# Kernel tuning notes

Measured on AMD Instinct MI355X. Metric: run time of the kernel, lower is better.

## Reference

```python
import jax, jax.numpy as jnp
from jax import lax
import numpy as np


def _gaussian_blur5(x):
    # x: [B,1,H,W]; torchvision gaussian_blur(kernel_size=5) default sigma = 0.3*((5-1)*0.5-1)+0.8 = 1.1
    sigma = 1.1
    r = jnp.arange(5, dtype=x.dtype) - 2.0
    k = jnp.exp(-(r * r) / (2.0 * sigma * sigma))
    k = k / k.sum()
    dn = ('NCHW', 'OIHW', 'NCHW')
    xp = jnp.pad(x, ((0, 0), (0, 0), (2, 2), (0, 0)), mode='reflect')
    x = lax.conv_general_dilated(xp, k.reshape(1, 1, 5, 1), (1, 1), 'VALID', dimension_numbers=dn)
    xp = jnp.pad(x, ((0, 0), (0, 0), (0, 0), (2, 2)), mode='reflect')
    return lax.conv_general_dilated(xp, k.reshape(1, 1, 1, 5), (1, 1), 'VALID', dimension_numbers=dn)


def setup_inputs() -> dict:
    key = jax.random.key(0)
    k1, k2, k3 = jax.random.split(key, 3)
    T, B, D, heads = 2, 32, 768, 12
    H_t, W_t, H_s, W_s = 14, 14, 96, 96
    template_patches = jax.random.normal(k1, (T, B, H_t * W_t, D), dtype=jnp.float32)
    template_annos = jax.random.uniform(k2, (T, B, 4), dtype=jnp.float32)
    search_key = jax.random.normal(k3, (B, heads, H_s * W_s + 1, D // heads), dtype=jnp.float32)
    return {'template_patches': template_patches, 'template_annos': template_annos,
            'search_key': search_key, 'H_t': H_t, 'W_t': W_t, 'H_s': H_s, 'W_s': W_s}


def reference(template_patches, template_annos, search_key, H_t, W_t, H_s, W_s):
    T, B, Nt, D = template_patches.shape
    heads = search_key.shape[1]
    hd = D // heads
    # --- vectorized patch-mask construction from normalized [x,y,w,h] boxes ---
    x1 = jnp.floor(template_annos[..., 0] * W_t).astype(jnp.int32)  # int() trunc == floor for >=0
    y1 = jnp.floor(template_annos[..., 1] * H_t).astype(jnp.int32)
    x2 = jnp.floor((template_annos[..., 0] + template_annos[..., 2]) * W_t).astype(jnp.int32)
    y2 = jnp.floor((template_annos[..., 1] + template_annos[..., 3]) * H_t).astype(jnp.int32)
    rows = jnp.arange(H_t)[None, None, :, None]
    cols = jnp.arange(W_t)[None, None, None, :]
    mask = ((rows >= y1[..., None, None]) & (rows < y2[..., None, None]) &
            (cols >= x1[..., None, None]) & (cols < x2[..., None, None]))
    mask = mask.reshape(T, B, Nt, 1).astype(template_patches.dtype)
    # --- masked-mean prototypes, averaged over templates ---
    count = mask.sum(axis=2)                                   # [T,B,1]
    protos = (template_patches * mask).sum(axis=2) / (count + 1e-6)  # [T,B,D]
    proto = protos.mean(axis=0)                                # [B,D]
    # --- per-head cross-attention scores against search keys (CLS stripped) ---
    proto_h = proto.reshape(B, heads, hd)
    skp = search_key[:, :, 1:, :]                              # [B,heads,Ns,hd]
    attn = jnp.einsum('bhd,bhnd->bhn', proto_h, skp) * (hd ** -0.5)
    track = attn.mean(axis=1).reshape(B, 1, H_s, W_s)
    track = _gaussian_blur5(track)
    prob = jax.nn.softmax(track.reshape(B, -1), axis=-1).reshape(B, H_s, W_s)
    # --- integral-image sliding-window box scoring ---
    im = jnp.cumsum(jnp.cumsum(prob, axis=-1), axis=-2)
    p = jnp.pad(im, ((0, 0), (1, 0), (1, 0)))
    Dv = p[:, H_t:, W_t:]
    Cv = p[:, H_t:, :-W_t]
    Bv = p[:, :-H_t, W_t:]
    Av = p[:, :-H_t, :-W_t]
    sum_map = Dv - Bv - Cv + Av                                # [B, H_s-H_t+1, W_s-W_t+1]
    flat = sum_map.reshape(B, -1)
    idx = jnp.argmax(flat, axis=1)
    confidence = jnp.max(flat, axis=1)
    best_y = idx // sum_map.shape[2]
    best_x = idx % sum_map.shape[2]
    win_w = jnp.full((B,), W_t, dtype=jnp.int32)
    win_h = jnp.full((B,), H_t, dtype=jnp.int32)
    return best_x, best_y, win_w, win_h, confidence, prob
```

## Files before the change

kernel.cpp:

```cpp
#include <hip/hip_runtime.h>
#include <math.h>

#define TT 2
#define BB 32
#define DD 768
#define HEADS 12
#define HD 64
#define HT 14
#define WT 14
#define HS 96
#define WS 96
#define NS (HS*WS)
#define NSK (NS+1)
#define SMW (WS-WT+1)
#define SMH (HS-HT+1)

__global__ __launch_bounds__(256) void proto_kernel(
    const float* __restrict__ patches, const float* __restrict__ annos,
    float* __restrict__ protos) {
  const int dc = blockIdx.x, t = blockIdx.y, b = blockIdx.z;
  const int d = dc * 256 + threadIdx.x;

  const float* an = annos + (t * BB + b) * 4;
  const float ax = an[0], ay = an[1], aw = an[2], ah = an[3];
  const int x1 = (int)floorf(ax * (float)WT);
  const int y1 = (int)floorf(ay * (float)HT);
  const int x2 = (int)floorf((ax + aw) * (float)WT);
  const int y2 = (int)floorf((ay + ah) * (float)HT);
  const int cx2 = min(x2, WT), cy2 = min(y2, HT);
  const int cw = max(cx2 - x1, 0), ch = max(cy2 - y1, 0);
  const float count = (float)(cw * ch);

  float s = 0.f;
  const float* base = patches + ((size_t)(t * BB + b)) * (HT*WT) * DD + d;
  for (int r = y1; r < cy2; ++r)
    for (int c = x1; c < cx2; ++c)
      s += base[(r * WT + c) * DD];

  protos[(size_t)(t * BB + b) * DD + d] = s / (count + 1e-6f);
}

__global__ __launch_bounds__(256) void attn_kernel(
    const float* __restrict__ sk, const float* __restrict__ protos,
    float* __restrict__ track) {
  const int b = blockIdx.y;
  const int tid = threadIdx.x;
  const int lane16 = tid & 15;
  const int grp = tid >> 4;
  const int n0 = blockIdx.x * 64;

  float4 pr[HEADS];
  const float4* p0 = (const float4*)(protos + (size_t)b * DD);
  const float4* p1 = (const float4*)(protos + (size_t)(BB + b) * DD);
  #pragma unroll
  for (int h = 0; h < HEADS; ++h) {
    float4 a = p0[h * 16 + lane16];
    float4 c = p1[h * 16 + lane16];
    pr[h] = make_float4(0.5f * (a.x + c.x), 0.5f * (a.y + c.y),
                        0.5f * (a.z + c.z), 0.5f * (a.w + c.w));
  }

  const float* skb = sk + (size_t)b * HEADS * NSK * HD;
  float acc[4] = {0.f, 0.f, 0.f, 0.f};
  #pragma unroll
  for (int j = 0; j < 4; ++j) {
    const int row = n0 + 16 * j + grp;
    const float4* base = (const float4*)(skb + (size_t)(row + 1) * HD) + lane16;
    #pragma unroll
    for (int h = 0; h < HEADS; ++h) {
      float4 v = base[h * (NSK * HD / 4)];
      acc[j] += v.x * pr[h].x + v.y * pr[h].y + v.z * pr[h].z + v.w * pr[h].w;
    }
  }

  #pragma unroll
  for (int j = 0; j < 4; ++j) {
    #pragma unroll
    for (int s = 1; s < 16; s <<= 1)
      acc[j] += __shfl_xor(acc[j], s, 64);
    if (lane16 == 0)
      track[(size_t)b * NS + n0 + 16 * j + grp] = acc[j] * (1.0f / 96.0f);
  }
}

__device__ __forceinline__ int reflect96(int p) {
  return p < 0 ? -p : (p > 95 ? 190 - p : p);
}

__global__ __launch_bounds__(256) void post_kernel(
    const float* __restrict__ track, float* __restrict__ out) {
  __shared__ float P[97 * 97];
  __shared__ float red[256];
  __shared__ int redi[256];
  const int b = blockIdx.x, tid = threadIdx.x;

  const float e2 = expf(-4.0f / (2.0f * 1.1f * 1.1f));
  const float e1 = expf(-1.0f / (2.0f * 1.1f * 1.1f));
  const float wsum = 2.f * e2 + 2.f * e1 + 1.f;
  const float w0 = e2 / wsum, w1 = e1 / wsum, w2 = 1.f / wsum;

  const float* tr = track + (size_t)b * NS;

  for (int i = tid; i < NS; i += 256) {
    const int r = i / WS, c = i % WS;
    float acc = w2 * tr[r * WS + c];
    acc += w1 * (tr[reflect96(r - 1) * WS + c] + tr[reflect96(r + 1) * WS + c]);
    acc += w0 * (tr[reflect96(r - 2) * WS + c] + tr[reflect96(r + 2) * WS + c]);
    P[r * 97 + c] = acc;
  }
  __syncthreads();

  float vals[36];
  #pragma unroll
  for (int k = 0; k < 36; ++k) {
    const int i = tid + k * 256;
    const int r = i / WS, c = i % WS;
    float acc = w2 * P[r * 97 + c];
    acc += w1 * (P[r * 97 + reflect96(c - 1)] + P[r * 97 + reflect96(c + 1)]);
    acc += w0 * (P[r * 97 + reflect96(c - 2)] + P[r * 97 + reflect96(c + 2)]);
    vals[k] = acc;
  }
  __syncthreads();

  float lm = -1e30f;
  #pragma unroll
  for (int k = 0; k < 36; ++k) lm = fmaxf(lm, vals[k]);
  red[tid] = lm; __syncthreads();
  for (int s = 128; s > 0; s >>= 1) {
    if (tid < s) red[tid] = fmaxf(red[tid], red[tid + s]);
    __syncthreads();
  }
  const float m = red[0]; __syncthreads();

  float ls = 0.f;
  #pragma unroll
  for (int k = 0; k < 36; ++k) { vals[k] = expf(vals[k] - m); ls += vals[k]; }
  red[tid] = ls; __syncthreads();
  for (int s = 128; s > 0; s >>= 1) {
    if (tid < s) red[tid] += red[tid + s];
    __syncthreads();
  }
  const float inv = 1.0f / red[0]; __syncthreads();

  float* prob_out = out + 5 * BB + (size_t)b * NS;
  #pragma unroll
  for (int k = 0; k < 36; ++k) {
    const int i = tid + k * 256;
    const int r = i / WS, c = i % WS;
    const float p = vals[k] * inv;
    prob_out[i] = p;
    P[(r + 1) * 97 + (c + 1)] = p;
  }
  for (int i = tid; i < 97; i += 256) { P[i] = 0.f; P[i * 97] = 0.f; }
  __syncthreads();

  if (tid < 96) {
    const int c = tid + 1;
    float run = P[97 + c];
    for (int r = 2; r < 97; ++r) { run += P[r * 97 + c]; P[r * 97 + c] = run; }
  }
  __syncthreads();
  if (tid < 96) {
    const int r = tid + 1;
    float run = 0.f;
    for (int c = 1; c < 97; ++c) { run += P[r * 97 + c]; P[r * 97 + c] = run; }
  }
  __syncthreads();

  float bv = -1e30f; int bi = 0x7fffffff;
  for (int i = tid; i < SMH * SMW; i += 256) {
    const int y = i / SMW, x = i % SMW;
    const float v = P[(y + HT) * 97 + (x + WT)] - P[y * 97 + (x + WT)]
                  - P[(y + HT) * 97 + x] + P[y * 97 + x];
    if (v > bv || (v == bv && i < bi)) { bv = v; bi = i; }
  }
  red[tid] = bv; redi[tid] = bi; __syncthreads();
  for (int s = 128; s > 0; s >>= 1) {
    if (tid < s) {
      const float ov = red[tid + s]; const int oi = redi[tid + s];
      if (ov > red[tid] || (ov == red[tid] && oi < redi[tid])) {
        red[tid] = ov; redi[tid] = oi;
      }
    }
    __syncthreads();
  }

  if (tid == 0) {
    const int idx = redi[0];
    out[0 * BB + b] = (float)(idx % SMW);
    out[1 * BB + b] = (float)(idx / SMW);
    out[2 * BB + b] = (float)WT;
    out[3 * BB + b] = (float)HT;
    out[4 * BB + b] = red[0];
  }
}

extern "C" void kernel_launch(void* const* d_in, const int* in_sizes, int n_in,
                              void* d_out, int out_size, void* d_ws, size_t ws_size,
                              hipStream_t stream) {
  (void)in_sizes; (void)n_in; (void)out_size; (void)ws_size;
  const float* patches = (const float*)d_in[0];
  const float* annos   = (const float*)d_in[1];
  const float* sk      = (const float*)d_in[2];
  float* ws = (float*)d_ws;
  float* protos = ws;
  float* track  = ws + (size_t)TT * BB * DD;
  float* out = (float*)d_out;

  proto_kernel<<<dim3(DD / 256, TT, BB), 256, 0, stream>>>(patches, annos, protos);
  attn_kernel<<<dim3(NS / 64, BB), 256, 0, stream>>>(sk, protos, track);
  post_kernel<<<BB, 256, 0, stream>>>(track, out);
}
```

Measured before the change: 1.199 ms.

## Parallelize attention per head with contiguous streaming and reduce heads in post kernel

Result: slower. 1.241 ms (+3.4%).

```diff
diff --git a/kernel.cpp b/kernel.cpp
--- a/kernel.cpp
+++ b/kernel.cpp
@@ -15,6 +15,10 @@
 #define SMW (WS-WT+1)
 #define SMH (HS-HT+1)
 
+#define CHUNKS 12
+#define CROWS (NS / CHUNKS)
+#define CITERS (CROWS / 16)
+
 __global__ __launch_bounds__(256) void proto_kernel(
     const float* __restrict__ patches, const float* __restrict__ annos,
     float* __restrict__ protos) {
@@ -40,46 +44,34 @@
   protos[(size_t)(t * BB + b) * DD + d] = s / (count + 1e-6f);
 }
 
-__global__ __launch_bounds__(256) void attn_kernel(
+__global__ __launch_bounds__(256, 8) void attn_kernel(
     const float* __restrict__ sk, const float* __restrict__ protos,
-    float* __restrict__ track) {
-  const int b = blockIdx.y;
+    float* __restrict__ track_h) {
+  const int chunk = blockIdx.x, h = blockIdx.y, b = blockIdx.z;
   const int tid = threadIdx.x;
   const int lane16 = tid & 15;
   const int grp = tid >> 4;
-  const int n0 = blockIdx.x * 64;
-
-  float4 pr[HEADS];
-  const float4* p0 = (const float4*)(protos + (size_t)b * DD);
-  const float4* p1 = (const float4*)(protos + (size_t)(BB + b) * DD);
-  #pragma unroll
-  for (int h = 0; h < HEADS; ++h) {
-    float4 a = p0[h * 16 + lane16];
-    float4 c = p1[h * 16 + lane16];
-    pr[h] = make_float4(0.5f * (a.x + c.x), 0.5f * (a.y + c.y),
-                        0.5f * (a.z + c.z), 0.5f * (a.w + c.w));
-  }
-
-  const float* skb = sk + (size_t)b * HEADS * NSK * HD;
-  float acc[4] = {0.f, 0.f, 0.f, 0.f};
-  #pragma unroll
-  for (int j = 0; j < 4; ++j) {
-    const int row = n0 + 16 * j + grp;
-    const float4* base = (const float4*)(skb + (size_t)(row + 1) * HD) + lane16;
-    #pragma unroll
-    for (int h = 0; h < HEADS; ++h) {
-      float4 v = base[h * (NSK * HD / 4)];
-      acc[j] += v.x * pr[h].x + v.y * pr[h].y + v.z * pr[h].z + v.w * pr[h].w;
-    }
-  }
-
-  #pragma unroll
-  for (int j = 0; j < 4; ++j) {
-    #pragma unroll
-    for (int s = 1; s < 16; s <<= 1)
-      acc[j] += __shfl_xor(acc[j], s, 64);
-    if (lane16 == 0)
-      track[(size_t)b * NS + n0 + 16 * j + grp] = acc[j] * (1.0f / 96.0f);
+
+  const float4* p0 = (const float4*)(protos + (size_t)b * DD + h * HD);
+  const float4* p1 = (const float4*)(protos + (size_t)(BB + b) * DD + h * HD);
+  const float4 a = p0[lane16], c = p1[lane16];
+  const float4 pr = make_float4(0.5f * (a.x + c.x), 0.5f * (a.y + c.y),
+                                0.5f * (a.z + c.z), 0.5f * (a.w + c.w));
+
+  const int row0 = chunk * CROWS;
+  const float4* base =
+      (const float4*)(sk + ((size_t)(b * HEADS + h) * NSK + 1 + row0) * HD);
+  float* outb = track_h + (size_t)(b * HEADS + h) * NS + row0;
+
+  #pragma unroll 8
+  for (int i = 0; i < CITERS; ++i) {
+    const float4 v = base[i * 256 + tid];
+    float r = v.x * pr.x + v.y * pr.y + v.z * pr.z + v.w * pr.w;
+    r += __shfl_xor(r, 1, 64);
+    r += __shfl_xor(r, 2, 64);
+    r += __shfl_xor(r, 4, 64);
+    r += __shfl_xor(r, 8, 64);
+    if (lane16 == 0) outb[i * 16 + grp] = r;
   }
 }
 
@@ -88,8 +80,9 @@
 }
 
 __global__ __launch_bounds__(256) void post_kernel(
-    const float* __restrict__ track, float* __restrict__ out) {
+    const float* __restrict__ track_h, float* __restrict__ out) {
   __shared__ float P[97 * 97];
+  __shared__ float Q[96 * 96];
   __shared__ float red[256];
   __shared__ int redi[256];
   const int b = blockIdx.x, tid = threadIdx.x;
@@ -99,13 +92,20 @@
   const float wsum = 2.f * e2 + 2.f * e1 + 1.f;
   const float w0 = e2 / wsum, w1 = e1 / wsum, w2 = 1.f / wsum;
 
-  const float* tr = track + (size_t)b * NS;
+  const float* trh = track_h + (size_t)b * HEADS * NS;
+  for (int i = tid; i < NS; i += 256) {
+    float s = 0.f;
+    #pragma unroll
+    for (int h = 0; h < HEADS; ++h) s += trh[h * NS + i];
+    Q[i] = s * (1.0f / 96.0f);
+  }
+  __syncthreads();
 
   for (int i = tid; i < NS; i += 256) {
     const int r = i / WS, c = i % WS;
-    float acc = w2 * tr[r * WS + c];
-    acc += w1 * (tr[reflect96(r - 1) * WS + c] + tr[reflect96(r + 1) * WS + c]);
-    acc += w0 * (tr[reflect96(r - 2) * WS + c] + tr[reflect96(r + 2) * WS + c]);
+    float acc = w2 * Q[r * WS + c];
+    acc += w1 * (Q[reflect96(r - 1) * WS + c] + Q[reflect96(r + 1) * WS + c]);
+    acc += w0 * (Q[reflect96(r - 2) * WS + c] + Q[reflect96(r + 2) * WS + c]);
     P[r * 97 + c] = acc;
   }
   __syncthreads();
@@ -203,11 +203,11 @@
   const float* annos   = (const float*)d_in[1];
   const float* sk      = (const float*)d_in[2];
   float* ws = (float*)d_ws;
-  float* protos = ws;
-  float* track  = ws + (size_t)TT * BB * DD;
+  float* protos  = ws;
+  float* track_h = ws + (size_t)TT * BB * DD;
   float* out = (float*)d_out;
 
   proto_kernel<<<dim3(DD / 256, TT, BB), 256, 0, stream>>>(patches, annos, protos);
-  attn_kernel<<<dim3(NS / 64, BB), 256, 0, stream>>>(sk, protos, track);
-  post_kernel<<<BB, 256, 0, stream>>>(track, out);
-}
+  attn_kernel<<<dim3(CHUNKS, HEADS, BB), 256, 0, stream>>>(sk, protos, track_h);
+  post_kernel<<<BB, 256, 0, stream>>>(track_h, out);
+}
```
